# Performance work log

Hardware: AMD Instinct MI355X
Metric: run time of the kernel (lower is better)

The kernel has to match this reference:

```python
import jax, jax.numpy as jnp
import numpy as np
import math

D_MODEL = 1024
NUM_HEADS = 16
D_K = D_MODEL // NUM_HEADS


def setup_inputs() -> dict:
    key = jax.random.key(0)
    ks = jax.random.split(key, 5)
    scale = 1.0 / math.sqrt(D_MODEL)
    x = jax.random.normal(ks[0], (2, 2048, D_MODEL), dtype=jnp.float32)
    qkv_w = jax.random.uniform(ks[1], (3 * D_MODEL, D_MODEL), jnp.float32, -scale, scale)
    qkv_b = jax.random.uniform(ks[2], (3 * D_MODEL,), jnp.float32, -scale, scale)
    out_w = jax.random.uniform(ks[3], (D_MODEL, D_MODEL), jnp.float32, -scale, scale)
    out_b = jax.random.uniform(ks[4], (D_MODEL,), jnp.float32, -scale, scale)
    return {"x": x, "qkv_w": qkv_w, "qkv_b": qkv_b, "out_w": out_w, "out_b": out_b}


def reference(x, qkv_w, qkv_b, out_w, out_b):
    B, N, D = x.shape
    # fused QKV projection (torch Linear: x @ W.T + b)
    qkv = x @ qkv_w.T + qkv_b                       # (B, N, 3D)
    qkv = qkv.reshape(B, N, 3, NUM_HEADS, D_K)
    qkv = jnp.transpose(qkv, (2, 0, 3, 1, 4))        # (3, B, H, N, d_k)
    q, k, v = qkv[0], qkv[1], qkv[2]
    attn = jnp.einsum('bhnd,bhmd->bhnm', q, k) / math.sqrt(D_K)  # (B,H,N,N)
    attn = jax.nn.softmax(attn, axis=-1)
    out = jnp.einsum('bhnm,bhmd->bhnd', attn, v)     # (B,H,N,d_k)
    out = jnp.transpose(out, (0, 2, 1, 3)).reshape(B, N, D)
    return out @ out_w.T + out_b
```

## Files before the change

### kernel.cpp

```cpp
#include <hip/hip_runtime.h>
#include <hip/hip_bf16.h>


typedef __bf16 bf16x8 __attribute__((ext_vector_type(8)));
typedef float f32x4 __attribute__((ext_vector_type(4)));

#define QSCALE 0.18033688011112042f

__device__ __forceinline__ unsigned short bfbits(float f) {
    union { __bf16 h; unsigned short u; } cv;
    cv.h = (__bf16)f;
    return cv.u;
}

__device__ __forceinline__ void gl_lds16(const void* g, void* l) {
    __builtin_amdgcn_global_load_lds(
        (__attribute__((address_space(1))) const unsigned int*)g,
        (__attribute__((address_space(3))) unsigned int*)l, 16, 0, 0);
}

__global__ void cvt_f32_bf16_v4(const float4* __restrict__ src,
                                ushort4* __restrict__ dst, int n4) {
    int i = blockIdx.x * blockDim.x + threadIdx.x;
    int stride = gridDim.x * blockDim.x;
    for (; i < n4; i += stride) {
        float4 f = src[i];
        ushort4 o;
        o.x = bfbits(f.x); o.y = bfbits(f.y); o.z = bfbits(f.z); o.w = bfbits(f.w);
        dst[i] = o;
    }
}

template<int MODE>
__global__ __launch_bounds__(256, 3) void gemm_mfma(
    const unsigned short* __restrict__ A,
    const unsigned short* __restrict__ W,
    const float* __restrict__ bias,
    unsigned short* __restrict__ qo,
    unsigned short* __restrict__ ko,
    unsigned short* __restrict__ vto,
    float* __restrict__ fo) {
    __shared__ __attribute__((aligned(128))) unsigned char smem[32768];
    const int lane = threadIdx.x & 63;
    const int w = threadIdx.x >> 6;
    const int g = lane >> 4, c = lane & 15;
    const int wr = w >> 1, wc = w & 1;
    const int row0 = blockIdx.x * 128;
    const int col0 = blockIdx.y * 128;

    const int rloc = lane >> 3;
    const int csrc = ((lane & 7) ^ rloc) * 8;

    f32x4 acc[4][4] = {};

    for (int kt = 0; kt < 1024; kt += 64) {
        #pragma unroll
        for (int i = 0; i < 4; ++i) {
            const int r = i * 32 + w * 8 + rloc;
            gl_lds16(A + (size_t)(row0 + r) * 1024 + kt + csrc,
                     smem + i * 4096 + w * 1024);
            gl_lds16(W + (size_t)(col0 + r) * 1024 + kt + csrc,
                     smem + 16384 + i * 4096 + w * 1024);
        }
        __syncthreads();

        #pragma unroll
        for (int ks = 0; ks < 2; ++ks) {
            bf16x8 a[4], b[4];
            #pragma unroll
            for (int mi = 0; mi < 4; ++mi) {
                const int r = wr * 64 + mi * 16 + c;
                a[mi] = *(const bf16x8*)(smem + r * 128 + (((ks * 4 + g) ^ (r & 7)) * 16));
            }
            #pragma unroll
            for (int ni = 0; ni < 4; ++ni) {
                const int r = wc * 64 + ni * 16 + c;
                b[ni] = *(const bf16x8*)(smem + 16384 + r * 128 + (((ks * 4 + g) ^ (r & 7)) * 16));
            }
            #pragma unroll
            for (int mi = 0; mi < 4; ++mi)
                #pragma unroll
                for (int ni = 0; ni < 4; ++ni)
                    acc[mi][ni] = __builtin_amdgcn_mfma_f32_16x16x32_bf16(
                        a[mi], b[ni], acc[mi][ni], 0, 0, 0);
        }
        __syncthreads();
    }

    #pragma unroll
    for (int mi = 0; mi < 4; ++mi) {
        #pragma unroll
        for (int ni = 0; ni < 4; ++ni) {
            const int col = col0 + wc * 64 + ni * 16 + c;
            const float bv = bias[col];
            #pragma unroll
            for (int j = 0; j < 4; ++j) {
                const int row = row0 + wr * 64 + mi * 16 + 4 * g + j;
                float v = acc[mi][ni][j] + bv;
                if (MODE == 1) {
                    fo[(size_t)row * 1024 + col] = v;
                } else {
                    const int sec = col >> 10;
                    const int d = col & 1023;
                    const int h = d >> 6, dk = d & 63;
                    const int b_ = row >> 11, n = row & 2047;
                    const int bh = b_ * 16 + h;
                    if (sec == 0)
                        qo[((size_t)(bh * 2048 + n) << 6) + dk] = bfbits(v * QSCALE);
                    else if (sec == 1)
                        ko[((size_t)(bh * 2048 + n) << 6) + dk] = bfbits(v);
                    else
                        vto[(size_t)(bh * 64 + dk) * 2048 + n] = bfbits(v);
                }
            }
        }
    }
}

__global__ __launch_bounds__(256, 4) void attn_flash(
    const unsigned short* __restrict__ Q,
    const unsigned short* __restrict__ K,
    const unsigned short* __restrict__ Vt,
    unsigned short* __restrict__ O) {
    __shared__ __attribute__((aligned(128))) unsigned char smem[40960];
    const int lane = threadIdx.x & 63;
    const int w = threadIdx.x >> 6;
    const int g = lane >> 4, c = lane & 15;
    const int c7 = c & 7;
    const int bh = blockIdx.y;
    const int q0 = blockIdx.x * 64 + w * 16;
    const unsigned short* Qb = Q + (size_t)bh * 2048 * 64;
    const unsigned short* Kb = K + (size_t)bh * 2048 * 64;
    const unsigned short* Vb = Vt + (size_t)bh * 64 * 2048;

    const int rloc = lane >> 3;
    const int csrc = ((lane & 7) ^ (rloc & 7)) * 8;

    const int chunkKV0 = ((0 + g) ^ c7) * 16;
    const int chunkKV1 = ((4 + g) ^ c7) * 16;

    unsigned char* Pbase = smem + 32768 + w * 2048;
    const int swzPc = (c ^ (c >> 3)) & 7;

    bf16x8 aq[2];
    #pragma unroll
    for (int ks = 0; ks < 2; ++ks)
        aq[ks] = *(const bf16x8*)(Qb + (size_t)(q0 + c) * 64 + ks * 32 + 8 * g);

    f32x4 o[4] = {};
    float m_run[4], l_run[4];
    #pragma unroll
    for (int j = 0; j < 4; ++j) { m_run[j] = -1e30f; l_run[j] = 0.f; }

    bf16x8 onesf;
    #pragma unroll
    for (int i = 0; i < 8; ++i) onesf[i] = (__bf16)1.0f;

    #pragma unroll
    for (int tt = 0; tt < 2; ++tt) {
        const int t = 2 * w + tt;
        const int row = 8 * t + rloc;
        gl_lds16(Kb + (size_t)row * 64 + csrc, smem + t * 1024);
        gl_lds16(Vb + (size_t)row * 2048 + csrc, smem + 16384 + t * 1024);
    }
    __syncthreads();

    int cur = 0;
    for (int kv = 0; kv < 2048; kv += 64) {
        if (kv + 64 < 2048) {
            const int nb = cur ^ 1;
            #pragma unroll
            for (int tt = 0; tt < 2; ++tt) {
                const int t = 2 * w + tt;
                const int row = 8 * t + rloc;
                gl_lds16(Kb + (size_t)(kv + 64 + row) * 64 + csrc,
                         smem + nb * 8192 + t * 1024);
                gl_lds16(Vb + (size_t)row * 2048 + (kv + 64) + csrc,
                         smem + 16384 + nb * 8192 + t * 1024);
            }
        }

        const unsigned char* Kt = smem + cur * 8192;
        const unsigned char* Vtb = smem + 16384 + cur * 8192;

        f32x4 s[4] = {};
        __builtin_amdgcn_s_setprio(1);
        #pragma unroll
        for (int nj = 0; nj < 4; ++nj) {
            bf16x8 bk0 = *(const bf16x8*)(Kt + nj * 2048 + c * 128 + chunkKV0);
            bf16x8 bk1 = *(const bf16x8*)(Kt + nj * 2048 + c * 128 + chunkKV1);
            s[nj] = __builtin_amdgcn_mfma_f32_16x16x32_bf16(aq[0], bk0, s[nj], 0, 0, 0);
            s[nj] = __builtin_amdgcn_mfma_f32_16x16x32_bf16(aq[1], bk1, s[nj], 0, 0, 0);
        }
        __builtin_amdgcn_s_setprio(0);

        float pmax[4];
        #pragma unroll
        for (int j = 0; j < 4; ++j)
            pmax[j] = fmaxf(fmaxf(s[0][j], s[1][j]), fmaxf(s[2][j], s[3][j]));

        const bool grow = (pmax[0] > m_run[0] + 8.f) || (pmax[1] > m_run[1] + 8.f) ||
                          (pmax[2] > m_run[2] + 8.f) || (pmax[3] > m_run[3] + 8.f);
        if (__any((int)grow)) {
            #pragma unroll
            for (int j = 0; j < 4; ++j) {
                float m0 = pmax[j];
                #pragma unroll
                for (int msk = 1; msk <= 8; msk <<= 1)
                    m0 = fmaxf(m0, __shfl_xor(m0, msk));
                const float mnew = fmaxf(m_run[j], m0);
                const float sc = __builtin_amdgcn_exp2f(m_run[j] - mnew);
                m_run[j] = mnew;
                l_run[j] *= sc;
                #pragma unroll
                for (int ni = 0; ni < 4; ++ni)
                    o[ni][j] *= sc;
            }
        }

        #pragma unroll
        for (int nj = 0; nj < 4; ++nj)
            #pragma unroll
            for (int j = 0; j < 4; ++j)
                s[nj][j] = __builtin_amdgcn_exp2f(s[nj][j] - m_run[j]);

        #pragma unroll
        for (int nj = 0; nj < 4; ++nj) {
            #pragma unroll
            for (int j = 0; j < 4; ++j) {
                const int r = 4 * g + j;
                const int swr = (r ^ (r >> 3)) & 7;
                *(unsigned short*)(Pbase + r * 128 + (((2 * nj + (c >> 3)) ^ swr) * 16) + c7 * 2)
                    = bfbits(s[nj][j]);
            }
        }

        f32x4 lt = {};
        __builtin_amdgcn_s_setprio(1);
        #pragma unroll
        for (int ks = 0; ks < 2; ++ks) {
            bf16x8 ap = *(const bf16x8*)(Pbase + c * 128 + (((ks * 4 + g) ^ swzPc) * 16));
            const int ck = ks ? chunkKV1 : chunkKV0;
            #pragma unroll
            for (int ni = 0; ni < 4; ++ni) {
                bf16x8 bv = *(const bf16x8*)(Vtb + ni * 2048 + c * 128 + ck);
                o[ni] = __builtin_amdgcn_mfma_f32_16x16x32_bf16(ap, bv, o[ni], 0, 0, 0);
            }
            lt = __builtin_amdgcn_mfma_f32_16x16x32_bf16(ap, onesf, lt, 0, 0, 0);
        }
        __builtin_amdgcn_s_setprio(0);
        #pragma unroll
        for (int j = 0; j < 4; ++j)
            l_run[j] += lt[j];

        __syncthreads();
        cur ^= 1;
    }

    const int b_ = bh >> 4, h = bh & 15;
    #pragma unroll
    for (int ni = 0; ni < 4; ++ni) {
        #pragma unroll
        for (int j = 0; j < 4; ++j) {
            const int row = b_ * 2048 + q0 + 4 * g + j;
            const int col = h * 64 + ni * 16 + c;
            O[(size_t)row * 1024 + col] = bfbits(o[ni][j] / l_run[j]);
        }
    }
}

extern "C" void kernel_launch(void* const* d_in, const int* in_sizes, int n_in,
                              void* d_out, int out_size, void* d_ws, size_t ws_size,
                              hipStream_t stream) {
    const float* x     = (const float*)d_in[0];
    const float* qkv_w = (const float*)d_in[1];
    const float* qkv_b = (const float*)d_in[2];
    const float* out_w = (const float*)d_in[3];
    const float* out_b = (const float*)d_in[4];
    float* out = (float*)d_out;

    char* ws = (char*)d_ws;
    unsigned short* xb   = (unsigned short*)(ws);
    unsigned short* wqkv = (unsigned short*)(ws + (8u  << 20));
    unsigned short* wout = (unsigned short*)(ws + (14u << 20));
    unsigned short* qb   = (unsigned short*)(ws + (16u << 20));
    unsigned short* kb   = (unsigned short*)(ws + (24u << 20));
    unsigned short* vtb  = (unsigned short*)(ws + (32u << 20));

    cvt_f32_bf16_v4<<<2048, 256, 0, stream>>>((const float4*)x,     (ushort4*)xb,   4096 * 1024 / 4);
    cvt_f32_bf16_v4<<<2048, 256, 0, stream>>>((const float4*)qkv_w, (ushort4*)wqkv, 3072 * 1024 / 4);
    cvt_f32_bf16_v4<<<1024, 256, 0, stream>>>((const float4*)out_w, (ushort4*)wout, 1024 * 1024 / 4);

    gemm_mfma<0><<<dim3(32, 24), 256, 0, stream>>>(xb, wqkv, qkv_b, qb, kb, vtb, nullptr);

    unsigned short* ao = xb;
    attn_flash<<<dim3(32, 32), 256, 0, stream>>>(qb, kb, vtb, ao);

    gemm_mfma<1><<<dim3(32, 8), 256, 0, stream>>>(ao, wout, out_b, nullptr, nullptr, nullptr, out);
}
```

Baseline: 136.2 us.

## Keep softmax probabilities in registers via transposed S MFMA, dropping LDS round-trip

Swaps the operand order of the QK^T MFMA so each lane holds a score column matching the A-operand layout of a 16x16x16 MFMA. The probabilities then feed the PV product directly from registers as bf16x4 instead of being written to and reread from a per-wave LDS buffer. The row max reduction becomes a per-lane max plus two cross-group shuffles, with the rescale factor broadcast by shuffle. This removes the P LDS stores and loads and 8 KB of shared memory, at the cost of twice as many smaller MFMAs for PV and narrower V loads from LDS.

After: 130.7 us. -4.0%, faster.

```diff
diff --git a/kernel.cpp b/kernel.cpp
--- a/kernel.cpp
+++ b/kernel.cpp
@@ -3,6 +3,8 @@
 
 
 typedef __bf16 bf16x8 __attribute__((ext_vector_type(8)));
+typedef __bf16 bf16x4 __attribute__((ext_vector_type(4)));
+typedef short short4v __attribute__((ext_vector_type(4)));
 typedef float f32x4 __attribute__((ext_vector_type(4)));
 
 #define QSCALE 0.18033688011112042f
@@ -11,6 +13,19 @@
     union { __bf16 h; unsigned short u; } cv;
     cv.h = (__bf16)f;
     return cv.u;
+}
+
+__device__ __forceinline__ f32x4 mfma16(bf16x4 a, bf16x4 b, f32x4 c) {
+#if __has_builtin(__builtin_amdgcn_mfma_f32_16x16x16bf16_1k)
+    union { bf16x4 h; short4v s; } ua, ub;
+    ua.h = a; ub.h = b;
+    return __builtin_amdgcn_mfma_f32_16x16x16bf16_1k(ua.s, ub.s, c, 0, 0, 0);
+#else
+    f32x4 d = c;
+    asm volatile("v_mfma_f32_16x16x16_bf16 %0, %1, %2, %0"
+                 : "+v"(d) : "v"(a), "v"(b));
+    return d;
+#endif
 }
 
 __device__ __forceinline__ void gl_lds16(const void* g, void* l) {
@@ -122,7 +137,7 @@
     const unsigned short* __restrict__ K,
     const unsigned short* __restrict__ Vt,
     unsigned short* __restrict__ O) {
-    __shared__ __attribute__((aligned(128))) unsigned char smem[40960];
+    __shared__ __attribute__((aligned(128))) unsigned char smem[32768];
     const int lane = threadIdx.x & 63;
     const int w = threadIdx.x >> 6;
     const int g = lane >> 4, c = lane & 15;
@@ -138,9 +153,8 @@
 
     const int chunkKV0 = ((0 + g) ^ c7) * 16;
     const int chunkKV1 = ((4 + g) ^ c7) * 16;
-
-    unsigned char* Pbase = smem + 32768 + w * 2048;
-    const int swzPc = (c ^ (c >> 3)) & 7;
+    const int ghalf = (g >> 1);
+    const int gsub = (g & 1) * 8;
 
     bf16x8 aq[2];
     #pragma unroll
@@ -148,13 +162,12 @@
         aq[ks] = *(const bf16x8*)(Qb + (size_t)(q0 + c) * 64 + ks * 32 + 8 * g);
 
     f32x4 o[4] = {};
-    float m_run[4], l_run[4];
-    #pragma unroll
-    for (int j = 0; j < 4; ++j) { m_run[j] = -1e30f; l_run[j] = 0.f; }
-
-    bf16x8 onesf;
-    #pragma unroll
-    for (int i = 0; i < 8; ++i) onesf[i] = (__bf16)1.0f;
+    f32x4 l_run = {};
+    float m_run = -1e30f;
+
+    bf16x4 ones4;
+    #pragma unroll
+    for (int i = 0; i < 4; ++i) ones4[i] = (__bf16)1.0f;
 
     #pragma unroll
     for (int tt = 0; tt < 2; ++tt) {
@@ -189,69 +202,56 @@
         for (int nj = 0; nj < 4; ++nj) {
             bf16x8 bk0 = *(const bf16x8*)(Kt + nj * 2048 + c * 128 + chunkKV0);
             bf16x8 bk1 = *(const bf16x8*)(Kt + nj * 2048 + c * 128 + chunkKV1);
-            s[nj] = __builtin_amdgcn_mfma_f32_16x16x32_bf16(aq[0], bk0, s[nj], 0, 0, 0);
-            s[nj] = __builtin_amdgcn_mfma_f32_16x16x32_bf16(aq[1], bk1, s[nj], 0, 0, 0);
+            s[nj] = __builtin_amdgcn_mfma_f32_16x16x32_bf16(bk0, aq[0], s[nj], 0, 0, 0);
+            s[nj] = __builtin_amdgcn_mfma_f32_16x16x32_bf16(bk1, aq[1], s[nj], 0, 0, 0);
         }
         __builtin_amdgcn_s_setprio(0);
 
-        float pmax[4];
-        #pragma unroll
-        for (int j = 0; j < 4; ++j)
-            pmax[j] = fmaxf(fmaxf(s[0][j], s[1][j]), fmaxf(s[2][j], s[3][j]));
-
-        const bool grow = (pmax[0] > m_run[0] + 8.f) || (pmax[1] > m_run[1] + 8.f) ||
-                          (pmax[2] > m_run[2] + 8.f) || (pmax[3] > m_run[3] + 8.f);
-        if (__any((int)grow)) {
+        float pmax = s[0][0];
+        #pragma unroll
+        for (int nj = 0; nj < 4; ++nj)
+            #pragma unroll
+            for (int j = 0; j < 4; ++j)
+                pmax = fmaxf(pmax, s[nj][j]);
+
+        if (__any((int)(pmax > m_run + 8.f))) {
+            float rm = pmax;
+            rm = fmaxf(rm, __shfl_xor(rm, 16));
+            rm = fmaxf(rm, __shfl_xor(rm, 32));
+            const float mnew = fmaxf(m_run, rm);
+            const float sc = __builtin_amdgcn_exp2f(m_run - mnew);
+            m_run = mnew;
             #pragma unroll
             for (int j = 0; j < 4; ++j) {
-                float m0 = pmax[j];
-                #pragma unroll
-                for (int msk = 1; msk <= 8; msk <<= 1)
-                    m0 = fmaxf(m0, __shfl_xor(m0, msk));
-                const float mnew = fmaxf(m_run[j], m0);
-                const float sc = __builtin_amdgcn_exp2f(m_run[j] - mnew);
-                m_run[j] = mnew;
-                l_run[j] *= sc;
+                const float scj = __shfl(sc, 4 * g + j);
+                l_run[j] *= scj;
                 #pragma unroll
                 for (int ni = 0; ni < 4; ++ni)
-                    o[ni][j] *= sc;
-            }
-        }
-
+                    o[ni][j] *= scj;
+            }
+        }
+
+        bf16x4 p[4];
         #pragma unroll
         for (int nj = 0; nj < 4; ++nj)
             #pragma unroll
             for (int j = 0; j < 4; ++j)
-                s[nj][j] = __builtin_amdgcn_exp2f(s[nj][j] - m_run[j]);
-
-        #pragma unroll
-        for (int nj = 0; nj < 4; ++nj) {
-            #pragma unroll
-            for (int j = 0; j < 4; ++j) {
-                const int r = 4 * g + j;
-                const int swr = (r ^ (r >> 3)) & 7;
-                *(unsigned short*)(Pbase + r * 128 + (((2 * nj + (c >> 3)) ^ swr) * 16) + c7 * 2)
-                    = bfbits(s[nj][j]);
-            }
-        }
+                p[nj][j] = (__bf16)__builtin_amdgcn_exp2f(s[nj][j] - m_run);
 
         f32x4 lt = {};
         __builtin_amdgcn_s_setprio(1);
         #pragma unroll
-        for (int ks = 0; ks < 2; ++ks) {
-            bf16x8 ap = *(const bf16x8*)(Pbase + c * 128 + (((ks * 4 + g) ^ swzPc) * 16));
-            const int ck = ks ? chunkKV1 : chunkKV0;
+        for (int nj = 0; nj < 4; ++nj) {
+            lt = mfma16(p[nj], ones4, lt);
             #pragma unroll
             for (int ni = 0; ni < 4; ++ni) {
-                bf16x8 bv = *(const bf16x8*)(Vtb + ni * 2048 + c * 128 + ck);
-                o[ni] = __builtin_amdgcn_mfma_f32_16x16x32_bf16(ap, bv, o[ni], 0, 0, 0);
-            }
-            lt = __builtin_amdgcn_mfma_f32_16x16x32_bf16(ap, onesf, lt, 0, 0, 0);
+                bf16x4 bv = *(const bf16x4*)(Vtb + (ni * 16 + c) * 128 +
+                                             (((2 * nj + ghalf) ^ c7) * 16) + gsub);
+                o[ni] = mfma16(p[nj], bv, o[ni]);
+            }
         }
         __builtin_amdgcn_s_setprio(0);
-        #pragma unroll
-        for (int j = 0; j < 4; ++j)
-            l_run[j] += lt[j];
+        l_run += lt;
 
         __syncthreads();
         cur ^= 1;
```
